# Optimization experiments

Hardware: AMD Instinct MI355X
Metric: run time of the kernel (lower is better)

Reference implementation:

```python
import jax, jax.numpy as jnp
import numpy as np

N, C, D, H, W = 1, 32, 64, 192, 160


def affine_grid_3d(theta, size):
    # PyTorch F.affine_grid 3D, align_corners=True convention.
    n, c, d, h, w = size
    z = jnp.linspace(-1.0, 1.0, d)
    y = jnp.linspace(-1.0, 1.0, h)
    x = jnp.linspace(-1.0, 1.0, w)
    zz, yy, xx = jnp.meshgrid(z, y, x, indexing='ij')          # [D,H,W]
    base = jnp.stack([xx, yy, zz, jnp.ones_like(xx)], axis=-1)  # [D,H,W,4]
    return jnp.einsum('dhwk,nck->ndhwc', base, theta)           # [N,D,H,W,3] (x,y,z)


def _gather_corner(vol, zi, yi, xi):
    # vol: [C,D,H,W]; zi/yi/xi: [D,H,W] int32. Zero padding outside.
    c, d, h, w = vol.shape
    valid = (zi >= 0) & (zi < d) & (yi >= 0) & (yi < h) & (xi >= 0) & (xi < w)
    zc = jnp.clip(zi, 0, d - 1)
    yc = jnp.clip(yi, 0, h - 1)
    xc = jnp.clip(xi, 0, w - 1)
    flat = vol.reshape(c, d * h * w)
    idx = (zc * h + yc) * w + xc
    vals = jnp.take(flat, idx.reshape(-1), axis=1).reshape(c, *zi.shape)
    return vals * valid[None].astype(vol.dtype)


def grid_sample_3d(inp, grid):
    # Trilinear grid_sample, zeros padding, align_corners=True.
    n, c, d, h, w = inp.shape
    x = (grid[..., 0] + 1.0) * 0.5 * (w - 1)
    y = (grid[..., 1] + 1.0) * 0.5 * (h - 1)
    z = (grid[..., 2] + 1.0) * 0.5 * (d - 1)
    x0 = jnp.floor(x).astype(jnp.int32); x1 = x0 + 1
    y0 = jnp.floor(y).astype(jnp.int32); y1 = y0 + 1
    z0 = jnp.floor(z).astype(jnp.int32); z1 = z0 + 1
    wx = (x - x0.astype(x.dtype))
    wy = (y - y0.astype(y.dtype))
    wz = (z - z0.astype(z.dtype))

    def sample_one(vol, z0, z1, y0, y1, x0, x1, wz, wy, wx):
        out = jnp.zeros((vol.shape[0],) + wz.shape, dtype=vol.dtype)
        for zi, wzc in ((z0, 1.0 - wz), (z1, wz)):
            for yi, wyc in ((y0, 1.0 - wy), (y1, wy)):
                for xi, wxc in ((x0, 1.0 - wx), (x1, wx)):
                    out = out + _gather_corner(vol, zi, yi, xi) * (wzc * wyc * wxc)[None]
        return out

    return jax.vmap(sample_one)(inp, z0, z1, y0, y1, x0, x1, wz, wy, wx)


def setup_inputs() -> dict:
    key = jax.random.key(0)
    k1, k2 = jax.random.split(key)
    inp = jax.random.normal(k1, (N, C, D, H, W), dtype=jnp.float32)
    identity = jnp.asarray([1, 0, 0, 0, 0, 1, 0, 0, 0, 0, 1, 0], dtype=jnp.float32)
    theta = identity + 0.1 * jax.random.normal(k2, (12,), dtype=jnp.float32)
    return {"input": inp, "theta": theta}


def reference(input, theta):
    th = theta.reshape(1, 3, 4)
    grid = affine_grid_3d(th, input.shape)       # [N,D,H,W,3]
    out = grid_sample_3d(input, grid)            # [N,C,D,H,W]
    return jnp.transpose(out, (0, 4, 3, 1, 2))   # [N,W,H,C,D]
```

## Files before the change

### kernel.cpp

```cpp
#include <hip/hip_runtime.h>

constexpr int W_ = 160;
constexpr int H_ = 192;
constexpr int D_ = 64;
constexpr int C_ = 32;
constexpr int HW_ = H_ * W_;
constexpr int DHW = D_ * H_ * W_;
constexpr int CD  = C_ * D_;

typedef float f4_t __attribute__((ext_vector_type(4)));

__global__ void __launch_bounds__(256)
affine_grid_sample_kernel(const float* __restrict__ inp,
                          const float* __restrict__ th,
                          float* __restrict__ out)
{
    __shared__ float lds[64 * 65];

    const int t    = threadIdx.x;
    const int lane = t & 63;
    const int sub  = t >> 6;

    const int bid = blockIdx.x;
    const int xcd = bid & 7;
    int local = bid >> 3;
    const int cs = local & 7;
    local >>= 3;
    const int wt = local % 3;
    const int r  = local / 3;
    const int hsub = r & 1;
    const int dt = r >> 1;
    const int h0 = xcd * 24 + hsub * 12;
    const int w0 = wt << 6;
    const int d0 = dt << 4;
    const int c0 = cs << 2;
    const int w  = w0 + lane;

    const float th0 = th[0], th1 = th[1], th2  = th[2],  th3  = th[3];
    const float th4 = th[4], th5 = th[5], th6  = th[6],  th7  = th[7];
    const float th8 = th[8], th9 = th[9], th10 = th[10], th11 = th[11];

    const float xx = fmaf((float)w, 2.0f / (W_ - 1), -1.0f);
    const unsigned mask = (w < W_) ? 0xFFFFFFFFu : 0u;

    const float* __restrict__ base = inp + (size_t)c0 * DHW;

    #pragma unroll 1
    for (int hl = 0; hl < 12; ++hl) {
        const int h = h0 + hl;
        const float yy = fmaf((float)h, 2.0f / (H_ - 1), -1.0f);

        unsigned offs[4][8];
        float u0a[4], u1a[4], v0a[4], v1a[4], s0a[4], s1a[4];

        #pragma unroll
        for (int k = 0; k < 4; ++k) {
            const int d = d0 + (sub << 2) + k;
            const float zz = fmaf((float)d, 2.0f / (D_ - 1), -1.0f);
            const float gx = fmaf(th0, xx, fmaf(th1, yy, fmaf(th2,  zz, th3)));
            const float gy = fmaf(th4, xx, fmaf(th5, yy, fmaf(th6,  zz, th7)));
            const float gz = fmaf(th8, xx, fmaf(th9, yy, fmaf(th10, zz, th11)));
            const float px = (gx + 1.0f) * (0.5f * (W_ - 1));
            const float py = (gy + 1.0f) * (0.5f * (H_ - 1));
            const float pz = (gz + 1.0f) * (0.5f * (D_ - 1));
            const float fx = floorf(px), fy = floorf(py), fz = floorf(pz);
            const int ix0 = (int)fx, iy0 = (int)fy, iz0 = (int)fz;
            const int ix1 = ix0 + 1, iy1 = iy0 + 1, iz1 = iz0 + 1;
            const float wx = px - fx, wy = py - fy, wz = pz - fz;
            u0a[k] = (ix0 >= 0 && ix0 < W_) ? (1.0f - wx) : 0.0f;
            u1a[k] = (ix1 >= 0 && ix1 < W_) ? wx          : 0.0f;
            v0a[k] = (iy0 >= 0 && iy0 < H_) ? (1.0f - wy) : 0.0f;
            v1a[k] = (iy1 >= 0 && iy1 < H_) ? wy          : 0.0f;
            s0a[k] = (iz0 >= 0 && iz0 < D_) ? (1.0f - wz) : 0.0f;
            s1a[k] = (iz1 >= 0 && iz1 < D_) ? wz          : 0.0f;
            const int cx0 = min(max(ix0, 0), W_ - 1), cx1 = min(max(ix1, 0), W_ - 1);
            const int cy0 = min(max(iy0, 0), H_ - 1), cy1 = min(max(iy1, 0), H_ - 1);
            const int cz0 = min(max(iz0, 0), D_ - 1), cz1 = min(max(iz1, 0), D_ - 1);
            const unsigned o00 = (unsigned)(cz0 * HW_ + cy0 * W_);
            const unsigned o01 = (unsigned)(cz0 * HW_ + cy1 * W_);
            const unsigned o10 = (unsigned)(cz1 * HW_ + cy0 * W_);
            const unsigned o11 = (unsigned)(cz1 * HW_ + cy1 * W_);
            offs[k][0] = (o00 + (unsigned)cx0) & mask;
            offs[k][1] = (o00 + (unsigned)cx1) & mask;
            offs[k][2] = (o01 + (unsigned)cx0) & mask;
            offs[k][3] = (o01 + (unsigned)cx1) & mask;
            offs[k][4] = (o10 + (unsigned)cx0) & mask;
            offs[k][5] = (o10 + (unsigned)cx1) & mask;
            offs[k][6] = (o11 + (unsigned)cx0) & mask;
            offs[k][7] = (o11 + (unsigned)cx1) & mask;
        }

        #pragma unroll
        for (int k = 0; k < 4; ++k) {
            const int ldsb = lane * 65 + ((sub << 2) + k) * 4;
            const float u0 = u0a[k], u1 = u1a[k];
            const float v0 = v0a[k], v1 = v1a[k];
            const float s0 = s0a[k], s1 = s1a[k];
            #pragma unroll
            for (int c = 0; c < 4; ++c) {
                const float* __restrict__ pc = base + (size_t)c * DHW;
                const float b000 = pc[offs[k][0]];
                const float b001 = pc[offs[k][1]];
                const float b010 = pc[offs[k][2]];
                const float b011 = pc[offs[k][3]];
                const float b100 = pc[offs[k][4]];
                const float b101 = pc[offs[k][5]];
                const float b110 = pc[offs[k][6]];
                const float b111 = pc[offs[k][7]];
                const float r00 = u0 * b000 + u1 * b001;
                const float r01 = u0 * b010 + u1 * b011;
                const float r10 = u0 * b100 + u1 * b101;
                const float r11 = u0 * b110 + u1 * b111;
                const float rz0 = v0 * r00 + v1 * r01;
                const float rz1 = v0 * r10 + v1 * r11;
                lds[ldsb + c] = s0 * rz0 + s1 * rz1;
            }
        }
        __syncthreads();

        {
            const int w2 = t >> 2;
            const int q  = t & 3;
            if (w0 + w2 < W_) {
                const int rb = w2 * 65 + q * 16;
                float* ob = out + ((size_t)(w0 + w2) * H_ + h) * CD
                                + (size_t)c0 * D_ + d0 + (q << 2);
                #pragma unroll
                for (int c = 0; c < 4; ++c) {
                    f4_t v;
                    v.x = lds[rb + 0  + c];
                    v.y = lds[rb + 4  + c];
                    v.z = lds[rb + 8  + c];
                    v.w = lds[rb + 12 + c];
                    __builtin_nontemporal_store(v, (f4_t*)(ob + (size_t)c * D_));
                }
            }
        }
        __syncthreads();
    }
}

extern "C" void kernel_launch(void* const* d_in, const int* in_sizes, int n_in,
                              void* d_out, int out_size, void* d_ws, size_t ws_size,
                              hipStream_t stream)
{
    const float* inp = (const float*)d_in[0];
    const float* th  = (const float*)d_in[1];
    float* out = (float*)d_out;

    hipLaunchKernelGGL(affine_grid_sample_kernel, dim3(1536), dim3(256), 0, stream,
                       inp, th, out);
}
```

Baseline: 776.5 us.

## Double-buffer LDS tile to drop second barrier and restructure gather per depth slice

Uses two LDS buffers that alternate each h iteration, so the barrier after the write-out phase can be removed and the next iteration's gathers can overlap the stores. The per-depth loop is fused so offsets are computed and all 32 corner loads issued per k before the blend, which lowers register pressure. It adds launch_bounds occupancy hint (4 blocks). Doubling LDS to about 33KB per block may limit occupancy, and the gathers are still issued in four separate batches.

```diff
diff --git a/kernel.cpp b/kernel.cpp
--- a/kernel.cpp
+++ b/kernel.cpp
@@ -10,12 +10,12 @@
 
 typedef float f4_t __attribute__((ext_vector_type(4)));
 
-__global__ void __launch_bounds__(256)
+__global__ void __launch_bounds__(256, 4)
 affine_grid_sample_kernel(const float* __restrict__ inp,
                           const float* __restrict__ th,
                           float* __restrict__ out)
 {
-    __shared__ float lds[64 * 65];
+    __shared__ float lds[2][64 * 65];
 
     const int t    = threadIdx.x;
     const int lane = t & 63;
@@ -45,13 +45,12 @@
 
     const float* __restrict__ base = inp + (size_t)c0 * DHW;
 
+    int buf = 0;
     #pragma unroll 1
     for (int hl = 0; hl < 12; ++hl) {
         const int h = h0 + hl;
         const float yy = fmaf((float)h, 2.0f / (H_ - 1), -1.0f);
-
-        unsigned offs[4][8];
-        float u0a[4], u1a[4], v0a[4], v1a[4], s0a[4], s1a[4];
+        float* __restrict__ L = lds[buf];
 
         #pragma unroll
         for (int k = 0; k < 4; ++k) {
@@ -67,12 +66,12 @@
             const int ix0 = (int)fx, iy0 = (int)fy, iz0 = (int)fz;
             const int ix1 = ix0 + 1, iy1 = iy0 + 1, iz1 = iz0 + 1;
             const float wx = px - fx, wy = py - fy, wz = pz - fz;
-            u0a[k] = (ix0 >= 0 && ix0 < W_) ? (1.0f - wx) : 0.0f;
-            u1a[k] = (ix1 >= 0 && ix1 < W_) ? wx          : 0.0f;
-            v0a[k] = (iy0 >= 0 && iy0 < H_) ? (1.0f - wy) : 0.0f;
-            v1a[k] = (iy1 >= 0 && iy1 < H_) ? wy          : 0.0f;
-            s0a[k] = (iz0 >= 0 && iz0 < D_) ? (1.0f - wz) : 0.0f;
-            s1a[k] = (iz1 >= 0 && iz1 < D_) ? wz          : 0.0f;
+            const float u0 = (ix0 >= 0 && ix0 < W_) ? (1.0f - wx) : 0.0f;
+            const float u1 = (ix1 >= 0 && ix1 < W_) ? wx          : 0.0f;
+            const float v0 = (iy0 >= 0 && iy0 < H_) ? (1.0f - wy) : 0.0f;
+            const float v1 = (iy1 >= 0 && iy1 < H_) ? wy          : 0.0f;
+            const float s0 = (iz0 >= 0 && iz0 < D_) ? (1.0f - wz) : 0.0f;
+            const float s1 = (iz1 >= 0 && iz1 < D_) ? wz          : 0.0f;
             const int cx0 = min(max(ix0, 0), W_ - 1), cx1 = min(max(ix1, 0), W_ - 1);
             const int cy0 = min(max(iy0, 0), H_ - 1), cy1 = min(max(iy1, 0), H_ - 1);
             const int cz0 = min(max(iz0, 0), D_ - 1), cz1 = min(max(iz1, 0), D_ - 1);
@@ -80,40 +79,35 @@
             const unsigned o01 = (unsigned)(cz0 * HW_ + cy1 * W_);
             const unsigned o10 = (unsigned)(cz1 * HW_ + cy0 * W_);
             const unsigned o11 = (unsigned)(cz1 * HW_ + cy1 * W_);
-            offs[k][0] = (o00 + (unsigned)cx0) & mask;
-            offs[k][1] = (o00 + (unsigned)cx1) & mask;
-            offs[k][2] = (o01 + (unsigned)cx0) & mask;
-            offs[k][3] = (o01 + (unsigned)cx1) & mask;
-            offs[k][4] = (o10 + (unsigned)cx0) & mask;
-            offs[k][5] = (o10 + (unsigned)cx1) & mask;
-            offs[k][6] = (o11 + (unsigned)cx0) & mask;
-            offs[k][7] = (o11 + (unsigned)cx1) & mask;
-        }
+            unsigned o[8];
+            o[0] = (o00 + (unsigned)cx0) & mask;
+            o[1] = (o00 + (unsigned)cx1) & mask;
+            o[2] = (o01 + (unsigned)cx0) & mask;
+            o[3] = (o01 + (unsigned)cx1) & mask;
+            o[4] = (o10 + (unsigned)cx0) & mask;
+            o[5] = (o10 + (unsigned)cx1) & mask;
+            o[6] = (o11 + (unsigned)cx0) & mask;
+            o[7] = (o11 + (unsigned)cx1) & mask;
 
-        #pragma unroll
-        for (int k = 0; k < 4; ++k) {
-            const int ldsb = lane * 65 + ((sub << 2) + k) * 4;
-            const float u0 = u0a[k], u1 = u1a[k];
-            const float v0 = v0a[k], v1 = v1a[k];
-            const float s0 = s0a[k], s1 = s1a[k];
+            float b[4][8];
             #pragma unroll
             for (int c = 0; c < 4; ++c) {
                 const float* __restrict__ pc = base + (size_t)c * DHW;
-                const float b000 = pc[offs[k][0]];
-                const float b001 = pc[offs[k][1]];
-                const float b010 = pc[offs[k][2]];
-                const float b011 = pc[offs[k][3]];
-                const float b100 = pc[offs[k][4]];
-                const float b101 = pc[offs[k][5]];
-                const float b110 = pc[offs[k][6]];
-                const float b111 = pc[offs[k][7]];
-                const float r00 = u0 * b000 + u1 * b001;
-                const float r01 = u0 * b010 + u1 * b011;
-                const float r10 = u0 * b100 + u1 * b101;
-                const float r11 = u0 * b110 + u1 * b111;
+                #pragma unroll
+                for (int j = 0; j < 8; ++j)
+                    b[c][j] = pc[o[j]];
+            }
+
+            const int ldsb = lane * 65 + ((sub << 2) + k) * 4;
+            #pragma unroll
+            for (int c = 0; c < 4; ++c) {
+                const float r00 = u0 * b[c][0] + u1 * b[c][1];
+                const float r01 = u0 * b[c][2] + u1 * b[c][3];
+                const float r10 = u0 * b[c][4] + u1 * b[c][5];
+                const float r11 = u0 * b[c][6] + u1 * b[c][7];
                 const float rz0 = v0 * r00 + v1 * r01;
                 const float rz1 = v0 * r10 + v1 * r11;
-                lds[ldsb + c] = s0 * rz0 + s1 * rz1;
+                L[ldsb + c] = s0 * rz0 + s1 * rz1;
             }
         }
         __syncthreads();
@@ -128,15 +122,15 @@
                 #pragma unroll
                 for (int c = 0; c < 4; ++c) {
                     f4_t v;
-                    v.x = lds[rb + 0  + c];
-                    v.y = lds[rb + 4  + c];
-                    v.z = lds[rb + 8  + c];
-                    v.w = lds[rb + 12 + c];
+                    v.x = L[rb + 0  + c];
+                    v.y = L[rb + 4  + c];
+                    v.z = L[rb + 8  + c];
+                    v.w = L[rb + 12 + c];
                     __builtin_nontemporal_store(v, (f4_t*)(ob + (size_t)c * D_));
                 }
             }
         }
-        __syncthreads();
+        buf ^= 1;
     }
 }
 
```

Result: faster. 743.9 us (-4.2%).
